# Performance work log

Hardware: AMD Instinct MI355X
Metric: run time of the kernel (lower is better)

## Reference

```python
import jax, jax.numpy as jnp
import numpy as np

D_MODEL = 512
N_HEADS = 8
NEG_INF = -1e9
LN_EPS = 1e-5


def setup_inputs() -> dict:
    key = jax.random.key(0)
    ks = jax.random.split(key, 8)
    B, V, T1, D = 8, 32, 192, D_MODEL
    T = T1 - 1
    x = jax.random.normal(ks[0], (B, V, T1, D), dtype=jnp.float32)
    obs_mask = jax.random.randint(ks[1], (B, V, T), 0, 2, dtype=jnp.int32)
    padding_mask = jax.random.randint(ks[2], (B, T), 0, 2) > 0
    s = 1.0 / np.sqrt(D)
    gamma = jnp.ones((D,), jnp.float32)
    beta = jnp.zeros((D,), jnp.float32)
    W_qkv = jax.random.normal(ks[3], (D, 3 * D), dtype=jnp.float32) * s
    W_proj = jax.random.normal(ks[4], (D, D), dtype=jnp.float32) * s
    b_proj = jnp.zeros((D,), jnp.float32)
    return {"x": x, "obs_mask": obs_mask, "padding_mask": padding_mask,
            "gamma": gamma, "beta": beta, "W_qkv": W_qkv,
            "W_proj": W_proj, "b_proj": b_proj}


def reference(x, obs_mask, padding_mask, gamma, beta, W_qkv, W_proj, b_proj):
    B, V, T1, D = x.shape
    H, dh = N_HEADS, D // N_HEADS
    BV = B * V

    x_flat = x.reshape(BV, T1, D)
    # LayerNorm (eval-mode dropout == identity)
    mu = jnp.mean(x_flat, axis=-1, keepdims=True)
    var = jnp.var(x_flat, axis=-1, keepdims=True)
    x_norm = (x_flat - mu) * jax.lax.rsqrt(var + LN_EPS) * gamma + beta

    qkv = (x_norm @ W_qkv).reshape(BV, T1, 3, H, dh)
    qkv = jnp.transpose(qkv, (2, 0, 3, 1, 4))  # (3, BV, H, T1, dh)
    q, k, v = qkv[0], qkv[1], qkv[2]

    # additive observation bias: mask[i] + mask[j] in {0,1,2}
    obs_ext = jnp.concatenate(
        [jnp.ones((B, V, 1), obs_mask.dtype), obs_mask], axis=2
    ).reshape(BV, T1).astype(jnp.float32)
    attn_bias = obs_ext[:, :, None] + obs_ext[:, None, :]  # (BV, T1, T1)

    # padding mask: True = valid; invalid pairs get -1e9
    pad_ext = jnp.concatenate(
        [jnp.ones((B, 1), bool), padding_mask], axis=1
    )  # (B, T1)
    pad_flat = jnp.broadcast_to(pad_ext[:, None, :], (B, V, T1)).reshape(BV, T1)
    pad_attn = pad_flat[:, :, None] & pad_flat[:, None, :]
    attn_bias = attn_bias + jnp.where(pad_attn, 0.0, NEG_INF)

    scale = 1.0 / jnp.sqrt(jnp.asarray(dh, jnp.float32))
    scores = jnp.einsum("bhqd,bhkd->bhqk", q, k) * scale + attn_bias[:, None]
    attn = jax.nn.softmax(scores, axis=-1)
    out = jnp.einsum("bhqk,bhkd->bhqd", attn, v)  # (BV, H, T1, dh)
    out = jnp.transpose(out, (0, 2, 1, 3)).reshape(BV, T1, D)
    out = out @ W_proj + b_proj
    return (x_flat + out).reshape(B, V, T1, D)
```

## Files before the change

### kernel.cpp

```cpp
#include <hip/hip_runtime.h>

#define DEVI __device__ __forceinline__

typedef __attribute__((ext_vector_type(8))) short short8;
typedef __attribute__((ext_vector_type(4))) float f32x4;

DEVI unsigned short f2bf(float f) {
  unsigned int u = __float_as_uint(f);
  u += 0x7fffu + ((u >> 16) & 1u);
  return (unsigned short)(u >> 16);
}

DEVI void gload16(const void* g, void* l) {
  __builtin_amdgcn_global_load_lds((__attribute__((address_space(1))) void*)g,
                                   (__attribute__((address_space(3))) void*)l, 16, 0, 0);
}

__global__ __launch_bounds__(256) void wprep(
    const float* __restrict__ Wq, const float* __restrict__ Wp,
    unsigned short* __restrict__ Wtq, unsigned short* __restrict__ Wtp) {
  int idx = blockIdx.x * 256 + threadIdx.x;
  int stride = gridDim.x * 256;
  for (int i = idx; i < 1536 * 512; i += stride) {
    int n = i >> 9, k = i & 511;
    Wtq[i] = f2bf(Wq[(size_t)k * 1536 + n]);
  }
  for (int i = idx; i < 512 * 512; i += stride) {
    int n = i >> 9, k = i & 511;
    Wtp[i] = f2bf(Wp[(size_t)k * 512 + n]);
  }
}

__global__ __launch_bounds__(256) void ln_kernel(
    const float* __restrict__ x, const float* __restrict__ gamma,
    const float* __restrict__ beta, unsigned short* __restrict__ xn) {
  int tid = threadIdx.x;
  int w = tid >> 6, l = tid & 63;
  size_t row = (size_t)blockIdx.x * 4 + w;
  const float* xr = x + row * 512 + l * 8;
  float4 v0 = *(const float4*)xr;
  float4 v1 = *(const float4*)(xr + 4);
  float s  = v0.x + v0.y + v0.z + v0.w + v1.x + v1.y + v1.z + v1.w;
  float ss = v0.x*v0.x + v0.y*v0.y + v0.z*v0.z + v0.w*v0.w
           + v1.x*v1.x + v1.y*v1.y + v1.z*v1.z + v1.w*v1.w;
  #pragma unroll
  for (int m = 1; m < 64; m <<= 1) {
    s  += __shfl_xor(s,  m);
    ss += __shfl_xor(ss, m);
  }
  float mean = s * (1.f / 512.f);
  float var  = ss * (1.f / 512.f) - mean * mean;
  float rstd = rsqrtf(var + 1e-5f);
  float4 g0 = *(const float4*)(gamma + l * 8);
  float4 g1 = *(const float4*)(gamma + l * 8 + 4);
  float4 b0 = *(const float4*)(beta + l * 8);
  float4 b1 = *(const float4*)(beta + l * 8 + 4);
  short8 ov;
  ov[0] = (short)f2bf((v0.x - mean) * rstd * g0.x + b0.x);
  ov[1] = (short)f2bf((v0.y - mean) * rstd * g0.y + b0.y);
  ov[2] = (short)f2bf((v0.z - mean) * rstd * g0.z + b0.z);
  ov[3] = (short)f2bf((v0.w - mean) * rstd * g0.w + b0.w);
  ov[4] = (short)f2bf((v1.x - mean) * rstd * g1.x + b1.x);
  ov[5] = (short)f2bf((v1.y - mean) * rstd * g1.y + b1.y);
  ov[6] = (short)f2bf((v1.z - mean) * rstd * g1.z + b1.z);
  ov[7] = (short)f2bf((v1.w - mean) * rstd * g1.w + b1.w);
  *(short8*)(xn + row * 512 + l * 8) = ov;
}

template<int EPI>
__global__ __launch_bounds__(256, 2) void gemm_bt(
    const unsigned short* __restrict__ A, const unsigned short* __restrict__ Bt,
    unsigned short* __restrict__ Cbf, float* __restrict__ Cf,
    const float* __restrict__ bias, const float* __restrict__ resid,
    int M, int N, int K) {
  __shared__ unsigned short As[128 * 64];
  __shared__ unsigned short Bs[128 * 64];
  int tid = threadIdx.x;
  int w = tid >> 6, l = tid & 63;
  int bn = blockIdx.x, bm = blockIdx.y;
  int wr = w >> 1, wc = w & 1;
  int t8 = tid >> 3, c8 = (tid & 7) * 8;
  int lr = l & 15, lk4 = l >> 4;
  const unsigned short* Ab = A + (size_t)bm * 128 * K;
  const unsigned short* Bb = Bt + (size_t)bn * 128 * K;
  f32x4 zero = {0.f, 0.f, 0.f, 0.f};
  f32x4 acc[4][4];
  #pragma unroll
  for (int i = 0; i < 4; i++)
    #pragma unroll
    for (int j = 0; j < 4; j++) acc[i][j] = zero;

  for (int k0 = 0; k0 < K; k0 += 64) {
    #pragma unroll
    for (int i = 0; i < 4; i++) {
      gload16(Ab + (size_t)(i * 32 + t8) * K + k0 + c8, (char*)As + i * 4096 + w * 1024);
      gload16(Bb + (size_t)(i * 32 + t8) * K + k0 + c8, (char*)Bs + i * 4096 + w * 1024);
    }
    __syncthreads();
    #pragma unroll
    for (int kk = 0; kk < 2; kk++) {
      short8 a[4], b[4];
      #pragma unroll
      for (int i = 0; i < 4; i++)
        a[i] = *(const short8*)&As[(wr * 64 + i * 16 + lr) * 64 + kk * 32 + lk4 * 8];
      #pragma unroll
      for (int j = 0; j < 4; j++)
        b[j] = *(const short8*)&Bs[(wc * 64 + j * 16 + lr) * 64 + kk * 32 + lk4 * 8];
      #pragma unroll
      for (int i = 0; i < 4; i++)
        #pragma unroll
        for (int j = 0; j < 4; j++)
          acc[i][j] = __builtin_amdgcn_mfma_f32_16x16x32_bf16(a[i], b[j], acc[i][j], 0, 0, 0);
    }
    __syncthreads();
  }
  int rb = bm * 128 + wr * 64 + lk4 * 4;
  int cb = bn * 128 + wc * 64 + lr;
  if (EPI == 0) {
    #pragma unroll
    for (int i = 0; i < 4; i++)
      #pragma unroll
      for (int j = 0; j < 4; j++)
        #pragma unroll
        for (int r = 0; r < 4; r++)
          Cbf[(size_t)(rb + i * 16 + r) * N + (cb + j * 16)] = f2bf(acc[i][j][r]);
  } else {
    #pragma unroll
    for (int i = 0; i < 4; i++)
      #pragma unroll
      for (int j = 0; j < 4; j++)
        #pragma unroll
        for (int r = 0; r < 4; r++) {
          int row = rb + i * 16 + r, col = cb + j * 16;
          Cf[(size_t)row * N + col] = acc[i][j][r] + bias[col] + resid[(size_t)row * N + col];
        }
  }
}

__global__ __launch_bounds__(256, 2) void attn_kernel(
    const unsigned short* __restrict__ qkv, unsigned short* __restrict__ aout,
    const int* __restrict__ obs_mask, const int* __restrict__ pad_mask) {
  const int LDQ = 72, LDV = 200, LDP = 104;
  __shared__ char smem[67072];
  unsigned short* Qs = (unsigned short*)smem;
  unsigned short* Ks = (unsigned short*)(smem + 27648);
  unsigned short* Vt = (unsigned short*)smem;
  unsigned short* Pw = (unsigned short*)(smem + 25600);
  float* obsb = (float*)(smem + 65536);
  int*   padb = (int*)(smem + 66304);

  int h = blockIdx.x, bv = blockIdx.y;
  int tid = threadIdx.x, w = tid >> 6, l = tid & 63;
  int lr = l & 15, lk4 = l >> 4;
  int b = bv >> 5;
  for (int t = tid; t < 192; t += 256) {
    obsb[t] = (t == 0) ? 1.f : (float)obs_mask[bv * 191 + (t - 1)];
    padb[t] = (t == 0) ? 1 : pad_mask[b * 191 + (t - 1)];
  }
  const unsigned short* base = qkv + (size_t)bv * 192 * 1536 + h * 64;
  for (int s = tid; s < 192 * 8; s += 256) {
    int row = s >> 3, c = (s & 7) * 8;
    *(short8*)&Qs[row * LDQ + c] = *(const short8*)(base + (size_t)row * 1536 + c);
    *(short8*)&Ks[row * LDQ + c] = *(const short8*)(base + (size_t)row * 1536 + 512 + c);
  }
  __syncthreads();
  f32x4 zero = {0.f, 0.f, 0.f, 0.f};
  f32x4 sc[3][12];
  #pragma unroll
  for (int i = 0; i < 3; i++)
    #pragma unroll
    for (int j = 0; j < 12; j++) sc[i][j] = zero;
  #pragma unroll
  for (int kk = 0; kk < 2; kk++) {
    short8 a[3], bb[12];
    #pragma unroll
    for (int i = 0; i < 3; i++)
      a[i] = *(const short8*)&Qs[(w * 48 + i * 16 + lr) * LDQ + kk * 32 + lk4 * 8];
    #pragma unroll
    for (int j = 0; j < 12; j++)
      bb[j] = *(const short8*)&Ks[(j * 16 + lr) * LDQ + kk * 32 + lk4 * 8];
    #pragma unroll
    for (int i = 0; i < 3; i++)
      #pragma unroll
      for (int j = 0; j < 12; j++)
        sc[i][j] = __builtin_amdgcn_mfma_f32_16x16x32_bf16(a[i], bb[j], sc[i][j], 0, 0, 0);
  }
  __syncthreads();

  for (int s = tid; s < 192 * 8; s += 256) {
    int row = s >> 3, d0 = (s & 7) * 8;
    short8 vv = *(const short8*)(base + (size_t)row * 1536 + 1024 + d0);
    int slot = ((d0 >> 3) & 7) << 4;
    #pragma unroll
    for (int e = 0; e < 8; e++) {
      int byte = (((d0 + e) * (LDV * 2) + row * 2) ^ slot);
      *(unsigned short*)((char*)Vt + byte) = (unsigned short)vv[e];
    }
  }
  float colobs[12];
  int colpad[12];
  #pragma unroll
  for (int j = 0; j < 12; j++) {
    colobs[j] = obsb[j * 16 + lr];
    colpad[j] = padb[j * 16 + lr];
  }
  #pragma unroll
  for (int i = 0; i < 3; i++) {
    #pragma unroll
    for (int r = 0; r < 4; r++) {
      int row = w * 48 + i * 16 + lk4 * 4 + r;
      float ro = obsb[row];
      int rp = padb[row];
      float vals[12];
      float mx = -3.0e38f;
      #pragma unroll
      for (int j = 0; j < 12; j++) {
        float vv = sc[i][j][r] * 0.125f + ro + colobs[j]
                 + ((rp & colpad[j]) ? 0.f : -1e9f);
        vals[j] = vv;
        mx = fmaxf(mx, vv);
      }
      #pragma unroll
      for (int m = 1; m < 16; m <<= 1) mx = fmaxf(mx, __shfl_xor(mx, m));
      float sum = 0.f;
      #pragma unroll
      for (int j = 0; j < 12; j++) {
        float e = __expf(vals[j] - mx);
        vals[j] = e;
        sum += e;
      }
      #pragma unroll
      for (int m = 1; m < 16; m <<= 1) sum += __shfl_xor(sum, m);
      float inv = 1.f / sum;
      #pragma unroll
      for (int j = 0; j < 12; j++) sc[i][j][r] = vals[j] * inv;
    }
  }
  __syncthreads();

  unsigned short* Pme = Pw + w * 48 * LDP;
  f32x4 o[3][4];
  #pragma unroll
  for (int i = 0; i < 3; i++)
    #pragma unroll
    for (int jd = 0; jd < 4; jd++) o[i][jd] = zero;
  #pragma unroll
  for (int kc = 0; kc < 2; kc++) {
    #pragma unroll
    for (int i = 0; i < 3; i++)
      #pragma unroll
      for (int r = 0; r < 4; r++) {
        int row = i * 16 + lk4 * 4 + r;
        #pragma unroll
        for (int jj = 0; jj < 6; jj++)
          Pme[row * LDP + jj * 16 + lr] = f2bf(sc[i][kc * 6 + jj][r]);
      }
    asm volatile("s_waitcnt lgkmcnt(0)" ::: "memory");
    __builtin_amdgcn_sched_barrier(0);
    #pragma unroll
    for (int kk = 0; kk < 3; kk++) {
      short8 a[3], bb[4];
      #pragma unroll
      for (int i = 0; i < 3; i++)
        a[i] = *(const short8*)&Pme[(i * 16 + lr) * LDP + kk * 32 + lk4 * 8];
      #pragma unroll
      for (int jd = 0; jd < 4; jd++) {
        int d = jd * 16 + lr;
        int byte = ((d * (LDV * 2) + (kc * 96 + kk * 32 + lk4 * 8) * 2) ^ (((d >> 3) & 7) << 4));
        bb[jd] = *(const short8*)((const char*)Vt + byte);
      }
      #pragma unroll
      for (int i = 0; i < 3; i++)
        #pragma unroll
        for (int jd = 0; jd < 4; jd++)
          o[i][jd] = __builtin_amdgcn_mfma_f32_16x16x32_bf16(a[i], bb[jd], o[i][jd], 0, 0, 0);
    }
  }
  unsigned short* ob = aout + (size_t)bv * 192 * 512 + h * 64;
  #pragma unroll
  for (int i = 0; i < 3; i++)
    #pragma unroll
    for (int jd = 0; jd < 4; jd++)
      #pragma unroll
      for (int r = 0; r < 4; r++) {
        int t = w * 48 + i * 16 + lk4 * 4 + r;
        int d = jd * 16 + lr;
        ob[(size_t)t * 512 + d] = f2bf(o[i][jd][r]);
      }
}

extern "C" void kernel_launch(void* const* d_in, const int* in_sizes, int n_in,
                              void* d_out, int out_size, void* d_ws, size_t ws_size,
                              hipStream_t stream) {
  const float* x     = (const float*)d_in[0];
  const int*   obs   = (const int*)d_in[1];
  const int*   pad   = (const int*)d_in[2];
  const float* gamma = (const float*)d_in[3];
  const float* beta  = (const float*)d_in[4];
  const float* Wq    = (const float*)d_in[5];
  const float* Wp    = (const float*)d_in[6];
  const float* bp    = (const float*)d_in[7];
  float* out = (float*)d_out;
  char* ws = (char*)d_ws;

  const size_t M = 49152;
  unsigned short* xn  = (unsigned short*)ws;
  unsigned short* qkv = (unsigned short*)(ws + M * 512 * 2);
  unsigned short* Wtq = (unsigned short*)(ws + M * 512 * 2 + M * 1536 * 2);
  unsigned short* Wtp = Wtq + 1536 * 512;

  wprep<<<dim3(512), dim3(256), 0, stream>>>(Wq, Wp, Wtq, Wtp);
  ln_kernel<<<dim3(12288), dim3(256), 0, stream>>>(x, gamma, beta, xn);
  gemm_bt<0><<<dim3(12, 384), dim3(256), 0, stream>>>(
      xn, Wtq, qkv, nullptr, nullptr, nullptr, 49152, 1536, 512);
  attn_kernel<<<dim3(8, 256), dim3(256), 0, stream>>>(qkv, xn, obs, pad);
  gemm_bt<1><<<dim3(4, 384), dim3(256), 0, stream>>>(
      xn, Wtp, nullptr, out, bp, x, 49152, 512, 512);
}
```

Baseline: 284.2 us.

## Swizzle GEMM LDS layout and remap workgroups across XCDs

Applies an XOR swizzle to the 16-byte chunks stored in shared memory for the bf16 GEMM tiles, so MFMA operand reads from rows sharing the same column spread across LDS banks. Also remaps the linear workgroup index so consecutive tiles land on the same XCD, aiming for better L2 reuse of A/B tiles. The swizzle adds a little address arithmetic. The remap assumes the workgroup count is divisible by eight.

```diff
diff --git a/kernel.cpp b/kernel.cpp
--- a/kernel.cpp
+++ b/kernel.cpp
@@ -72,14 +72,19 @@
     const unsigned short* __restrict__ A, const unsigned short* __restrict__ Bt,
     unsigned short* __restrict__ Cbf, float* __restrict__ Cf,
     const float* __restrict__ bias, const float* __restrict__ resid,
-    int M, int N, int K) {
+    int M, int N, int K, int nbx) {
   __shared__ unsigned short As[128 * 64];
   __shared__ unsigned short Bs[128 * 64];
   int tid = threadIdx.x;
   int w = tid >> 6, l = tid & 63;
-  int bn = blockIdx.x, bm = blockIdx.y;
+  int nwg = nbx * gridDim.y;
+  int lin = blockIdx.y * nbx + blockIdx.x;
+  int cpx = nwg >> 3;
+  int swz = (lin & 7) * cpx + (lin >> 3);
+  int bn = swz % nbx, bm = swz / nbx;
   int wr = w >> 1, wc = w & 1;
-  int t8 = tid >> 3, c8 = (tid & 7) * 8;
+  int t8 = tid >> 3;
+  int c8s = (((tid & 7) ^ ((tid >> 3) & 7)) * 8);
   int lr = l & 15, lk4 = l >> 4;
   const unsigned short* Ab = A + (size_t)bm * 128 * K;
   const unsigned short* Bb = Bt + (size_t)bn * 128 * K;
@@ -93,19 +98,25 @@
   for (int k0 = 0; k0 < K; k0 += 64) {
     #pragma unroll
     for (int i = 0; i < 4; i++) {
-      gload16(Ab + (size_t)(i * 32 + t8) * K + k0 + c8, (char*)As + i * 4096 + w * 1024);
-      gload16(Bb + (size_t)(i * 32 + t8) * K + k0 + c8, (char*)Bs + i * 4096 + w * 1024);
+      gload16(Ab + (size_t)(i * 32 + t8) * K + k0 + c8s, (char*)As + i * 4096 + w * 1024);
+      gload16(Bb + (size_t)(i * 32 + t8) * K + k0 + c8s, (char*)Bs + i * 4096 + w * 1024);
     }
     __syncthreads();
     #pragma unroll
     for (int kk = 0; kk < 2; kk++) {
       short8 a[4], b[4];
       #pragma unroll
-      for (int i = 0; i < 4; i++)
-        a[i] = *(const short8*)&As[(wr * 64 + i * 16 + lr) * 64 + kk * 32 + lk4 * 8];
-      #pragma unroll
-      for (int j = 0; j < 4; j++)
-        b[j] = *(const short8*)&Bs[(wc * 64 + j * 16 + lr) * 64 + kk * 32 + lk4 * 8];
+      for (int i = 0; i < 4; i++) {
+        int ra = wr * 64 + i * 16 + lr;
+        a[i] = *(const short8*)((const char*)As + ra * 128 +
+                                (((kk * 64 + lk4 * 16)) ^ ((ra & 7) << 4)));
+      }
+      #pragma unroll
+      for (int j = 0; j < 4; j++) {
+        int rb = wc * 64 + j * 16 + lr;
+        b[j] = *(const short8*)((const char*)Bs + rb * 128 +
+                                (((kk * 64 + lk4 * 16)) ^ ((rb & 7) << 4)));
+      }
       #pragma unroll
       for (int i = 0; i < 4; i++)
         #pragma unroll
@@ -312,8 +323,8 @@
   wprep<<<dim3(512), dim3(256), 0, stream>>>(Wq, Wp, Wtq, Wtp);
   ln_kernel<<<dim3(12288), dim3(256), 0, stream>>>(x, gamma, beta, xn);
   gemm_bt<0><<<dim3(12, 384), dim3(256), 0, stream>>>(
-      xn, Wtq, qkv, nullptr, nullptr, nullptr, 49152, 1536, 512);
+      xn, Wtq, qkv, nullptr, nullptr, nullptr, 49152, 1536, 512, 12);
   attn_kernel<<<dim3(8, 256), dim3(256), 0, stream>>>(qkv, xn, obs, pad);
   gemm_bt<1><<<dim3(4, 384), dim3(256), 0, stream>>>(
-      xn, Wtp, nullptr, out, bp, x, 49152, 512, 512);
-}
+      xn, Wtp, nullptr, out, bp, x, 49152, 512, 512, 4);
+}
```

New measurement: 260.1 us. 8.5% less time.
